# Kernel tuning notes

Measured on AMD Instinct MI355X. Metric: run time of the kernel, lower is better.

Reference implementation:

```python
import jax, jax.numpy as jnp
import numpy as np

# Circuit structure constants (match init_kwargs)
N_NODES = 32768        # number of sum nodes in this layer
N_CHILD = 65536        # number of child nodes
NNZ = 1048576          # number of sparse weight entries (avg fan-in 32)
BATCH = 128


def setup_inputs() -> dict:
    key = jax.random.key(0)
    k1, k2, k3, k4 = jax.random.split(key, 4)
    # child log-likelihoods per sample (output of child layers)
    child_ll = jax.random.normal(k1, (BATCH, N_CHILD), dtype=jnp.float32)
    # sparse log-weights of the BCOO weight matrix [N_NODES, N_CHILD]
    log_w = jax.random.normal(k2, (NNZ,), dtype=jnp.float32)
    rows = jnp.sort(jax.random.randint(k3, (NNZ,), 0, N_NODES)).astype(jnp.int64)
    cols = jax.random.randint(k4, (NNZ,), 0, N_CHILD).astype(jnp.int64)
    return {"child_ll": child_ll, "log_w": log_w, "rows": rows, "cols": cols}


def reference(child_ll, log_w, rows, cols):
    """Faithful jax translation of SumLayer.log_likelihood_of_nodes.

    Original: per sample, exponentiate BCOO log-weights and child
    log-likelihoods, sparse matvec (weights @ exp(child_ll)), then
    log(result) - log_normalization_constants, where the normalization
    constants are log(row-sums of exp(log_weights)).
    """
    w = jnp.exp(log_w)  # [NNZ]
    # log normalization constants: log of row-sums of exp(log_weights)
    log_z = jnp.log(jax.ops.segment_sum(w, rows, num_segments=N_NODES))  # [N_NODES]

    def per_sample(ll):  # ll: [N_CHILD]
        p = jnp.exp(ll)
        contrib = w * p[cols]                                   # gather + weight [NNZ]
        return jax.ops.segment_sum(contrib, rows, num_segments=N_NODES)  # [N_NODES]

    s = jax.vmap(per_sample)(child_ll)  # [BATCH, N_NODES]
    return jnp.log(s) - log_z
```

## Files before the change

### kernel.cpp

```cpp
#include <hip/hip_runtime.h>
#include <hip/hip_fp16.h>
#include <math.h>

#define BATCH     128
#define N_NODES   32768
#define N_CHILD   65536
#define NNZ_TOTAL 1048576
#define NMAX      64

__global__ __launch_bounds__(256) void exp_transpose_kernel(
    const float* __restrict__ child_ll, __half* __restrict__ ex) {
    __shared__ float tile[64][BATCH + 1];
    const int c0 = blockIdx.x * 64;
    const int t  = threadIdx.x;

    {
        const int cl = t & 63;
        const int b0 = t >> 6;
#pragma unroll
        for (int j = 0; j < BATCH / 4; ++j) {
            const int b = b0 + j * 4;
            tile[cl][b] = expf(child_ll[(size_t)b * N_CHILD + c0 + cl]);
        }
    }
    __syncthreads();

    {
        const int cl = t >> 5;
        const int b0 = (t & 31) * 4;
#pragma unroll
        for (int p = 0; p < 8; ++p) {
            const int c = p * 8 + cl;
            union { __half2 h[2]; uint2 u; } pack;
            pack.h[0] = __half2{__float2half(tile[c][b0]),     __float2half(tile[c][b0 + 1])};
            pack.h[1] = __half2{__float2half(tile[c][b0 + 2]), __float2half(tile[c][b0 + 3])};
            *(uint2*)&ex[(size_t)(c0 + c) * BATCH + b0] = pack.u;
        }
    }
}

__global__ __launch_bounds__(256) void exp_w_kernel(
    const float* __restrict__ log_w, float* __restrict__ w) {
    const int i = (blockIdx.x * 256 + threadIdx.x) * 4;
    float4 v = *(const float4*)&log_w[i];
    v.x = expf(v.x); v.y = expf(v.y); v.z = expf(v.z); v.w = expf(v.w);
    *(float4*)&w[i] = v;
}

__global__ __launch_bounds__(256) void row_starts_kernel(
    const int* __restrict__ rows, int* __restrict__ row_start) {
    const int r = blockIdx.x * blockDim.x + threadIdx.x;
    if (r > N_NODES) return;
    if (r == N_NODES) { row_start[r] = NNZ_TOTAL; return; }
    int lo = 0, hi = NNZ_TOTAL;
    while (lo < hi) {
        const int mid = (lo + hi) >> 1;
        if (rows[mid] < r) lo = mid + 1; else hi = mid;
    }
    row_start[r] = lo;
}

__global__ __launch_bounds__(256, 4) void sum_rows_kernel(
    const __half* __restrict__ ex, const float* __restrict__ w,
    const int* __restrict__ cols, const int* __restrict__ row_start,
    float* __restrict__ out) {
    const int wave = threadIdx.x >> 6;
    const int lane = threadIdx.x & 63;
    const int bid  = blockIdx.x;
    const int rb   = (bid & 7) * (N_NODES / 4 / 8) + (bid >> 3);
    const int r    = rb * 4 + wave;

    const int start = row_start[r];
    const int end   = row_start[r + 1];
    const int b0    = lane * 2;

    float accx = 0.f, accy = 0.f, wsum = 0.f;

    for (int base = start; base < end; base += NMAX) {
        const int idx  = base + lane;
        const bool v   = idx < end;
        const int   c  = __builtin_nontemporal_load(&cols[min(idx, NNZ_TOTAL - 1)]);
        const float wv = v ? __builtin_nontemporal_load(&w[idx]) : 0.f;
        const int  seg = min(end - base, NMAX);

        __half2 g[NMAX];
#pragma unroll
        for (int j = 0; j < NMAX; ++j) {
            const int cj = __builtin_amdgcn_readlane(c, j);
            g[j] = *(const __half2*)&ex[((size_t)(unsigned)cj << 7) + b0];
        }

#pragma unroll
        for (int jb = 0; jb < NMAX; jb += 16) {
            if (jb >= seg) break;
#pragma unroll
            for (int jj = 0; jj < 16; ++jj) {
                const int j = jb + jj;
                const float wj = __uint_as_float(
                    __builtin_amdgcn_readlane(__float_as_uint(wv), j));
                const float2 f = __half22float2(g[j]);
                accx += wj * f.x;
                accy += wj * f.y;
                wsum += wj;
            }
        }
    }

    const float logz = logf(wsum);
    out[(size_t)b0 * N_NODES + r]       = logf(accx) - logz;
    out[(size_t)(b0 + 1) * N_NODES + r] = logf(accy) - logz;
}

extern "C" void kernel_launch(void* const* d_in, const int* in_sizes, int n_in,
                              void* d_out, int out_size, void* d_ws, size_t ws_size,
                              hipStream_t stream) {
    const float* child_ll = (const float*)d_in[0];
    const float* log_w    = (const float*)d_in[1];
    const int*   rows     = (const int*)d_in[2];
    const int*   cols     = (const int*)d_in[3];
    float*       out      = (float*)d_out;

    __half* ex        = (__half*)d_ws;
    float*  w         = (float*)((char*)d_ws + (size_t)N_CHILD * BATCH * 2);
    int*    row_start = (int*)((char*)w + (size_t)NNZ_TOTAL * 4);

    exp_transpose_kernel<<<N_CHILD / 64, 256, 0, stream>>>(child_ll, ex);
    exp_w_kernel<<<NNZ_TOTAL / 1024, 256, 0, stream>>>(log_w, w);
    row_starts_kernel<<<(N_NODES + 256) / 256 + 1, 256, 0, stream>>>(rows, row_start);
    sum_rows_kernel<<<N_NODES / 4, 256, 0, stream>>>(ex, w, cols, row_start, out);
}
```

Before: 69.29 us.

## Software-pipeline sparse row gathers in 16-entry chunks, shuffle-reduce weight sum

The sum kernel now issues gathers in 16-entry chunks and double-buffers them: the next chunk's loads are issued before the current chunk's FMAs. This replaces the old scheme that loaded all 64 gathers up front, so far fewer registers are live at once and loads overlap with arithmetic without gathering for segments that are absent. The weight sum is now accumulated per lane and reduced with a cross-lane shuffle instead of a scalar-broadcast add inside the inner loop. The transpose kernel now stores 16-byte vectors instead of 8-byte ones. The chunk conditionals and the register copies between buffers add some control and move overhead.

```diff
diff --git a/kernel.cpp b/kernel.cpp
--- a/kernel.cpp
+++ b/kernel.cpp
@@ -6,7 +6,6 @@
 #define N_NODES   32768
 #define N_CHILD   65536
 #define NNZ_TOTAL 1048576
-#define NMAX      64
 
 __global__ __launch_bounds__(256) void exp_transpose_kernel(
     const float* __restrict__ child_ll, __half* __restrict__ ex) {
@@ -26,15 +25,17 @@
     __syncthreads();
 
     {
-        const int cl = t >> 5;
-        const int b0 = (t & 31) * 4;
+        const int cl = t >> 4;
+        const int b0 = (t & 15) * 8;
 #pragma unroll
-        for (int p = 0; p < 8; ++p) {
-            const int c = p * 8 + cl;
-            union { __half2 h[2]; uint2 u; } pack;
-            pack.h[0] = __half2{__float2half(tile[c][b0]),     __float2half(tile[c][b0 + 1])};
-            pack.h[1] = __half2{__float2half(tile[c][b0 + 2]), __float2half(tile[c][b0 + 3])};
-            *(uint2*)&ex[(size_t)(c0 + c) * BATCH + b0] = pack.u;
+        for (int p = 0; p < 4; ++p) {
+            const int c = p * 16 + cl;
+            union { __half2 h[4]; uint4 u; } pk;
+#pragma unroll
+            for (int k = 0; k < 4; ++k)
+                pk.h[k] = __half2{__float2half(tile[c][b0 + 2 * k]),
+                                  __float2half(tile[c][b0 + 2 * k + 1])};
+            *(uint4*)&ex[(size_t)(c0 + c) * BATCH + b0] = pk.u;
         }
     }
 }
@@ -72,43 +73,62 @@
 
     const int start = row_start[r];
     const int end   = row_start[r + 1];
-    const int b0    = lane * 2;
+    const char* exb = (const char*)ex;
+    const unsigned bo = (unsigned)lane * 4u;
 
-    float accx = 0.f, accy = 0.f, wsum = 0.f;
+    float accx = 0.f, accy = 0.f, wlane = 0.f;
 
-    for (int base = start; base < end; base += NMAX) {
-        const int idx  = base + lane;
-        const bool v   = idx < end;
-        const int   c  = __builtin_nontemporal_load(&cols[min(idx, NNZ_TOTAL - 1)]);
-        const float wv = v ? __builtin_nontemporal_load(&w[idx]) : 0.f;
-        const int  seg = min(end - base, NMAX);
+    for (int base = start; base < end; base += 64) {
+        const int  idx   = base + lane;
+        const bool valid = idx < end;
+        const int  cidx  = valid ? idx : start;
+        const int  c     = __builtin_nontemporal_load(&cols[cidx]);
+        const float wv   = valid ? __builtin_nontemporal_load(&w[idx]) : 0.f;
+        wlane += wv;
+        const int seg = end - base;
 
-        __half2 g[NMAX];
+        __half2 ga[16], gb[16];
+
 #pragma unroll
-        for (int j = 0; j < NMAX; ++j) {
-            const int cj = __builtin_amdgcn_readlane(c, j);
-            g[j] = *(const __half2*)&ex[((size_t)(unsigned)cj << 7) + b0];
+        for (int jj = 0; jj < 16; ++jj) {
+            const unsigned cj = (unsigned)__builtin_amdgcn_readlane(c, jj);
+            ga[jj] = *(const __half2*)(exb + ((size_t)cj << 8) + bo);
         }
 
 #pragma unroll
-        for (int jb = 0; jb < NMAX; jb += 16) {
-            if (jb >= seg) break;
+        for (int t16 = 0; t16 < 4; ++t16) {
+            if (t16 < 3 && (t16 + 1) * 16 < seg) {
 #pragma unroll
-            for (int jj = 0; jj < 16; ++jj) {
-                const int j = jb + jj;
-                const float wj = __uint_as_float(
-                    __builtin_amdgcn_readlane(__float_as_uint(wv), j));
-                const float2 f = __half22float2(g[j]);
-                accx += wj * f.x;
-                accy += wj * f.y;
-                wsum += wj;
+                for (int jj = 0; jj < 16; ++jj) {
+                    const int j = (t16 + 1) * 16 + jj;
+                    const unsigned cj = (unsigned)__builtin_amdgcn_readlane(c, j);
+                    gb[jj] = *(const __half2*)(exb + ((size_t)cj << 8) + bo);
+                }
             }
+            if (t16 * 16 < seg) {
+#pragma unroll
+                for (int jj = 0; jj < 16; ++jj) {
+                    const int j = t16 * 16 + jj;
+                    const float wj = __uint_as_float(
+                        __builtin_amdgcn_readlane(__float_as_uint(wv), j));
+                    const __half2 g = ga[jj];
+                    accx = fmaf(wj, __half2float(__low2half(g)), accx);
+                    accy = fmaf(wj, __half2float(__high2half(g)), accy);
+                }
+            }
+#pragma unroll
+            for (int jj = 0; jj < 16; ++jj) ga[jj] = gb[jj];
         }
     }
 
+    float wsum = wlane;
+#pragma unroll
+    for (int m = 1; m < 64; m <<= 1) wsum += __shfl_xor(wsum, m, 64);
     const float logz = logf(wsum);
-    out[(size_t)b0 * N_NODES + r]       = logf(accx) - logz;
-    out[(size_t)(b0 + 1) * N_NODES + r] = logf(accy) - logz;
+
+    const int b = lane * 2;
+    out[(size_t)b * N_NODES + r]       = logf(accx) - logz;
+    out[(size_t)(b + 1) * N_NODES + r] = logf(accy) - logz;
 }
 
 extern "C" void kernel_launch(void* const* d_in, const int* in_sizes, int n_in,
```

Result: faster. 67.44 us (-2.7%).
